# Kernel tuning notes

Measured on AMD Instinct MI355X. Metric: run time of the kernel, lower is better.

## Reference

```python
import jax, jax.numpy as jnp
import numpy as np

G = 128        # number of graphs
N = 512        # nodes per graph
F_IN = 128     # n_feat
H = 128        # agg_hidden
L = 5          # n_layer
FC = 128       # fc_hidden
C = 10         # n_class
E_HALF = 8192  # undirected edge pairs per graph (symmetrized -> 16384 directed)


def setup_inputs() -> dict:
    key = jax.random.key(0)
    ks = jax.random.split(key, 8)
    x = jax.random.normal(ks[0], (G * N, F_IN), dtype=jnp.float32)
    # per-graph random edges, offset into the block-diagonal node index space
    s = jax.random.randint(ks[1], (G, E_HALF), 0, N)
    d = jax.random.randint(ks[2], (G, E_HALF), 0, N)
    off = (jnp.arange(G) * N)[:, None]
    s = (s + off).reshape(-1)
    d = (d + off).reshape(-1)
    src = jnp.concatenate([s, d])  # symmetric adjacency (edges + reversed)
    dst = jnp.concatenate([d, s])
    eps = jnp.zeros((L,), jnp.float32)  # nn.Parameter(torch.zeros(n_layer))
    W = jax.random.normal(ks[3], (L, H, H), jnp.float32) / jnp.sqrt(H)
    b = jnp.zeros((L, H), jnp.float32)
    fc1_w = jax.random.normal(ks[4], (H, FC), jnp.float32) / jnp.sqrt(H)
    fc1_b = jnp.zeros((FC,), jnp.float32)
    fc2_w = jax.random.normal(ks[5], (FC, C), jnp.float32) / jnp.sqrt(FC)
    fc2_b = jnp.zeros((C,), jnp.float32)
    return {"x": x, "eps": eps, "W": W, "b": b,
            "fc1_w": fc1_w, "fc1_b": fc1_b, "fc2_w": fc2_w, "fc2_b": fc2_b,
            "src": src, "dst": dst}


def reference(x, eps, W, b, fc1_w, fc1_b, fc2_w, fc2_b, src, dst):
    n = x.shape[0]
    h = x
    for i in range(L):
        # sparse Adj @ h : gather along src, scatter-add to dst
        pooled = jax.ops.segment_sum(h[src], dst, num_segments=n)
        h = jax.nn.relu(((1.0 + eps[i]) * h + pooled) @ W[i] + b[i])
        # dropout p=0.0 / eval mode -> identity
    hg = h.reshape(G, N, -1).sum(axis=1)          # sum readout over nodes
    hg = jax.nn.relu(hg @ fc1_w + fc1_b)
    return jax.nn.softmax(hg @ fc2_w + fc2_b, axis=-1)
```

## Files before the change

kernel.cpp:

```cpp
#include <hip/hip_runtime.h>

#define GNUM  128
#define NPG   512
#define FDIM  128

#define OFF_A   0u
#define OFF_WT  (16u<<20)
#define OFF_HTA (17u<<20)
#define OFF_HTB (33u<<20)

typedef short bf16x8 __attribute__((ext_vector_type(8)));
typedef float f32x4  __attribute__((ext_vector_type(4)));
typedef unsigned short u16;

#define GLB_AS __attribute__((address_space(1)))
#define LDS_AS __attribute__((address_space(3)))

static __device__ inline void gload16(const void* g, void* l) {
    __builtin_amdgcn_global_load_lds((const GLB_AS unsigned*)g,
                                     (LDS_AS unsigned*)l, 16, 0, 0);
}

static __device__ inline unsigned bf1(float x) {
    unsigned b = __float_as_uint(x);
    return (b + 0x7fffu + ((b >> 16) & 1u)) >> 16;
}
static __device__ inline unsigned pack_bf2(float x, float y) {
    return bf1(x) | (bf1(y) << 16);
}
static __device__ inline bf16x8 cvt8n(unsigned x) {
    union { bf16x8 v; unsigned u[4]; } r;
#pragma unroll
    for (int i = 0; i < 4; ++i) {
        float f0 = (float)((x >> (8 * i)) & 0xFu);
        float f1 = (float)((x >> (8 * i + 4)) & 0xFu);
        r.u[i] = (__float_as_uint(f0) >> 16) | (__float_as_uint(f1) & 0xffff0000u);
    }
    return r.v;
}

__global__ __launch_bounds__(256) void k_prep(const float* __restrict__ x,
                                              u16* __restrict__ hT,
                                              const float* __restrict__ W,
                                              u16* __restrict__ wt) {
    __shared__ char Cs[128 * 144];
    int t = threadIdx.x;
    int bid = blockIdx.x;
    if (bid >= 1024) {
        int idx = (bid - 1024) * 256 + t;
        int l = idx >> 14, r = idx & 16383;
        int n = r >> 7, k = r & 127;
        wt[idx] = (u16)bf1(W[(l << 14) + k * 128 + n]);
        return;
    }
    int m0 = bid * 64;
    int g = m0 >> 9, ml0 = m0 & 511;
#pragma unroll
    for (int it = 0; it < 8; ++it) {
        int i = t + 256 * it;
        int nl = i >> 5, fq = i & 31;
        float4 v = *(const float4*)(x + (size_t)(m0 + nl) * FDIM + fq * 4);
        *(u16*)(Cs + (fq * 4 + 0) * 144 + nl * 2) = (u16)bf1(v.x);
        *(u16*)(Cs + (fq * 4 + 1) * 144 + nl * 2) = (u16)bf1(v.y);
        *(u16*)(Cs + (fq * 4 + 2) * 144 + nl * 2) = (u16)bf1(v.z);
        *(u16*)(Cs + (fq * 4 + 3) * 144 + nl * 2) = (u16)bf1(v.w);
    }
    __syncthreads();
    u16* hg = hT + (size_t)g * 65536 + ml0;
#pragma unroll
    for (int j = 0; j < 4; ++j) {
        int idx = t + 256 * j;
        int f = idx >> 3, piece = idx & 7;
        uint4 v = *(const uint4*)(Cs + f * 144 + piece * 16);
        *(uint4*)((char*)(hg + (size_t)f * 512) + piece * 16) = v;
    }
}

__global__ __launch_bounds__(1024) void k_adense(const int* __restrict__ src,
                                                 const int* __restrict__ dst,
                                                 unsigned* __restrict__ A4,
                                                 int halfE) {
    __shared__ uint4 cnt4[512 * 16];
    unsigned* cnt = (unsigned*)cnt4;
    int g = blockIdx.x;
    int t = threadIdx.x;
#pragma unroll
    for (int j = 0; j < 8; ++j) cnt4[t + 1024 * j] = make_uint4(0u, 0u, 0u, 0u);
    __syncthreads();
    int epg = halfE / GNUM;
#pragma unroll
    for (int r = 0; r < 2; ++r) {
        int base = r * halfE + g * epg;
        const int4* s4 = (const int4*)(src + base);
        const int4* d4 = (const int4*)(dst + base);
#pragma unroll
        for (int it = 0; it < 2; ++it) {
            int i = t + 1024 * it;
            int4 sv = s4[i], dv = d4[i];
            int s, d;
            s = sv.x & 511; d = dv.x & 511; atomicAdd(&cnt[d * 64 + (s >> 3)], 1u << ((s & 7) * 4));
            s = sv.y & 511; d = dv.y & 511; atomicAdd(&cnt[d * 64 + (s >> 3)], 1u << ((s & 7) * 4));
            s = sv.z & 511; d = dv.z & 511; atomicAdd(&cnt[d * 64 + (s >> 3)], 1u << ((s & 7) * 4));
            s = sv.w & 511; d = dv.w & 511; atomicAdd(&cnt[d * 64 + (s >> 3)], 1u << ((s & 7) * 4));
        }
    }
    __syncthreads();
    uint4* Ao = (uint4*)(A4 + (size_t)g * 512 * 64);
#pragma unroll
    for (int j = 0; j < 8; ++j) Ao[t + 1024 * j] = cnt4[t + 1024 * j];
}

__global__ __launch_bounds__(512, 2) void k_layer(const u16* __restrict__ hT,
                                                  u16* __restrict__ hTo,
                                                  const unsigned char* __restrict__ A,
                                                  const u16* __restrict__ wt,
                                                  const float* __restrict__ bias,
                                                  const float* __restrict__ eps) {
    __shared__ uint4 smem16[118784 / 16];
    char* smem = (char*)smem16;
    char* Ps = smem + 49152;
    int t = threadIdx.x;
    int w = t >> 6, lane = t & 63;
    int q = lane >> 4, ln = lane & 15;
    int g = blockIdx.x & 127, hf = blockIdx.x >> 7;
    const unsigned char* Ab = A + (size_t)g * 131072 + (size_t)hf * 65536;
    const u16* hb = hT + (size_t)g * 65536;
    int rA0 = w * 32 + ln;

    unsigned aA[32];
#pragma unroll
    for (int ch = 0; ch < 8; ++ch)
#pragma unroll
        for (int kcL = 0; kcL < 2; ++kcL)
#pragma unroll
            for (int h = 0; h < 2; ++h)
                aA[ch * 4 + kcL * 2 + h] = *(const unsigned*)
                    (Ab + (size_t)(rA0 + h * 16) * 256 + ch * 32 + kcL * 16 + q * 4);

    f32x4 acc[2][8];
#pragma unroll
    for (int mt = 0; mt < 2; ++mt)
#pragma unroll
        for (int nt = 0; nt < 8; ++nt) acc[mt][nt] = (f32x4){0.f, 0.f, 0.f, 0.f};

#pragma unroll
    for (int c = 0; c < 2; ++c)
#pragma unroll
        for (int j = 0; j < 2; ++j) {
            int p = t + 512 * j; int f = p >> 3;
            gload16((const char*)hb + (size_t)f * 1024 + c * 128
                        + (((p & 7) ^ (f & 7)) << 4),
                    smem + c * 16384 + p * 16);
        }
#pragma unroll
    for (int ch = 0; ch < 8; ++ch) {
        char* Bsc = smem + (ch % 3) * 16384;
        if (ch < 6) {
            int cn = ch + 2;
            char* Bsn = smem + (cn % 3) * 16384;
#pragma unroll
            for (int j = 0; j < 2; ++j) {
                int p = t + 512 * j; int f = p >> 3;
                gload16((const char*)hb + (size_t)f * 1024 + cn * 128
                            + (((p & 7) ^ (f & 7)) << 4),
                        Bsn + p * 16);
            }
        }
        if (ch < 6)      asm volatile("s_waitcnt vmcnt(4)" ::: "memory");
        else if (ch < 7) asm volatile("s_waitcnt vmcnt(2)" ::: "memory");
        else             asm volatile("s_waitcnt vmcnt(0)" ::: "memory");
        __builtin_amdgcn_s_barrier();
#pragma unroll
        for (int kcL = 0; kcL < 2; ++kcL) {
            bf16x8 af0 = cvt8n(aA[ch * 4 + kcL * 2 + 0]);
            bf16x8 af1 = cvt8n(aA[ch * 4 + kcL * 2 + 1]);
#pragma unroll
            for (int nt = 0; nt < 8; ++nt) {
                int f = nt * 16 + ln;
                int sB = f * 8 + ((kcL * 4 + q) ^ (f & 7));
                bf16x8 bf = *(const bf16x8*)(Bsc + sB * 16);
                acc[0][nt] = __builtin_amdgcn_mfma_f32_16x16x32_bf16(af0, bf, acc[0][nt], 0, 0, 0);
                acc[1][nt] = __builtin_amdgcn_mfma_f32_16x16x32_bf16(af1, bf, acc[1][nt], 0, 0, 0);
            }
        }
        __builtin_amdgcn_s_barrier();
    }
    float ep = 1.f + eps[0];
#pragma unroll
    for (int mt = 0; mt < 2; ++mt) {
        int rl0 = w * 32 + mt * 16 + q * 4;
        int mb0 = hf * 256 + rl0;
#pragma unroll
        for (int nt = 0; nt < 8; ++nt) {
            int f = nt * 16 + ln;
            uint2 sv = *(const uint2*)(hb + (size_t)f * 512 + mb0);
            float s0 = __uint_as_float(sv.x << 16);
            float s1 = __uint_as_float(sv.x & 0xffff0000u);
            float s2 = __uint_as_float(sv.y << 16);
            float s3 = __uint_as_float(sv.y & 0xffff0000u);
            f32x4 a = acc[mt][nt];
            *(u16*)(Ps + (rl0 + 0) * 272 + f * 2) = (u16)bf1(fmaf(ep, s0, a[0]));
            *(u16*)(Ps + (rl0 + 1) * 272 + f * 2) = (u16)bf1(fmaf(ep, s1, a[1]));
            *(u16*)(Ps + (rl0 + 2) * 272 + f * 2) = (u16)bf1(fmaf(ep, s2, a[2]));
            *(u16*)(Ps + (rl0 + 3) * 272 + f * 2) = (u16)bf1(fmaf(ep, s3, a[3]));
        }
    }
    __syncthreads();
    f32x4 acc2[2][8];
#pragma unroll
    for (int mt = 0; mt < 2; ++mt)
#pragma unroll
        for (int nt = 0; nt < 8; ++nt) acc2[mt][nt] = (f32x4){0.f, 0.f, 0.f, 0.f};
#pragma unroll
    for (int ks = 0; ks < 4; ++ks) {
        bf16x8 af0 = *(const bf16x8*)(Ps + rA0 * 272 + ks * 64 + q * 16);
        bf16x8 af1 = *(const bf16x8*)(Ps + (rA0 + 16) * 272 + ks * 64 + q * 16);
#pragma unroll
        for (int nt = 0; nt < 8; ++nt) {
            bf16x8 bf = *(const bf16x8*)(wt + (size_t)(nt * 16 + ln) * 128 + ks * 32 + q * 8);
            acc2[0][nt] = __builtin_amdgcn_mfma_f32_16x16x32_bf16(af0, bf, acc2[0][nt], 0, 0, 0);
            acc2[1][nt] = __builtin_amdgcn_mfma_f32_16x16x32_bf16(af1, bf, acc2[1][nt], 0, 0, 0);
        }
    }
    __syncthreads();
#pragma unroll
    for (int mt = 0; mt < 2; ++mt) {
        int rl0 = w * 32 + mt * 16 + q * 4;
#pragma unroll
        for (int nt = 0; nt < 8; ++nt) {
            int n = nt * 16 + ln;
            float bv = bias[n];
            f32x4 a = acc2[mt][nt];
            *(uint2*)(Ps + n * 528 + rl0 * 2) =
                make_uint2(pack_bf2(fmaxf(a[0] + bv, 0.f), fmaxf(a[1] + bv, 0.f)),
                           pack_bf2(fmaxf(a[2] + bv, 0.f), fmaxf(a[3] + bv, 0.f)));
        }
    }
    __syncthreads();
    u16* ho = hTo + (size_t)g * 65536 + hf * 256;
#pragma unroll
    for (int j = 0; j < 8; ++j) {
        int idx = t + 512 * j;
        int f = idx >> 5, piece = idx & 31;
        uint4 v = *(const uint4*)(Ps + f * 528 + piece * 16);
        *(uint4*)((char*)(ho + (size_t)f * 512) + piece * 16) = v;
    }
}

__global__ __launch_bounds__(128) void k_r(const u16* __restrict__ hT,
                                           const float* __restrict__ fc1w,
                                           const float* __restrict__ fc1b,
                                           const float* __restrict__ fc2w,
                                           const float* __restrict__ fc2b,
                                           float* __restrict__ out) {
    __shared__ float hg[128], z[128], lg[10];
    int g = blockIdx.x, t = threadIdx.x;
    const uint4* row = (const uint4*)(hT + (size_t)g * 65536 + (size_t)t * 512);
    float acc = 0.f;
#pragma unroll 4
    for (int i = 0; i < 64; ++i) {
        uint4 u = row[i];
        acc += __uint_as_float(u.x << 16) + __uint_as_float(u.x & 0xffff0000u);
        acc += __uint_as_float(u.y << 16) + __uint_as_float(u.y & 0xffff0000u);
        acc += __uint_as_float(u.z << 16) + __uint_as_float(u.z & 0xffff0000u);
        acc += __uint_as_float(u.w << 16) + __uint_as_float(u.w & 0xffff0000u);
    }
    hg[t] = acc;
    __syncthreads();
    float a1 = fc1b[t];
#pragma unroll 4
    for (int k = 0; k < 128; ++k) a1 = fmaf(hg[k], fc1w[k * 128 + t], a1);
    z[t] = fmaxf(a1, 0.f);
    __syncthreads();
    if (t < 10) {
        float l2 = fc2b[t];
        for (int k = 0; k < 128; ++k) l2 = fmaf(z[k], fc2w[k * 10 + t], l2);
        lg[t] = l2;
    }
    __syncthreads();
    if (t < 10) {
        float m = lg[0];
        for (int c = 1; c < 10; ++c) m = fmaxf(m, lg[c]);
        float ssum = 0.f;
        for (int c = 0; c < 10; ++c) ssum += expf(lg[c] - m);
        out[g * 10 + t] = expf(lg[t] - m) / ssum;
    }
}

extern "C" void kernel_launch(void* const* d_in, const int* in_sizes, int n_in,
                              void* d_out, int out_size, void* d_ws, size_t ws_size,
                              hipStream_t stream) {
    const float* x    = (const float*)d_in[0];
    const float* eps  = (const float*)d_in[1];
    const float* W    = (const float*)d_in[2];
    const float* b    = (const float*)d_in[3];
    const float* fc1w = (const float*)d_in[4];
    const float* fc1b = (const float*)d_in[5];
    const float* fc2w = (const float*)d_in[6];
    const float* fc2b = (const float*)d_in[7];
    const int*   src  = (const int*)d_in[8];
    const int*   dst  = (const int*)d_in[9];
    int E = in_sizes[8];
    int halfE = E >> 1;

    char* ws  = (char*)d_ws;
    unsigned char* Abuf = (unsigned char*)(ws + OFF_A);
    u16*  wtb = (u16*)(ws + OFF_WT);
    u16*  hta = (u16*)(ws + OFF_HTA);
    u16*  htb = (u16*)(ws + OFF_HTB);
    float* out = (float*)d_out;

    k_prep<<<1344, 256, 0, stream>>>(x, hta, W, wtb);
    k_adense<<<GNUM, 1024, 0, stream>>>(src, dst, (unsigned*)Abuf, halfE);

    u16* cur = hta;
    u16* nxt = htb;
    for (int l = 0; l < 5; ++l) {
        k_layer<<<GNUM * 2, 512, 0, stream>>>(cur, nxt, Abuf,
                                              wtb + l * 128 * 128, b + l * 128, eps + l);
        u16* tmp = cur; cur = nxt; nxt = tmp;
    }
    k_r<<<GNUM, 128, 0, stream>>>(cur, fc1w, fc1b, fc2w, fc2b, out);
}
```

Measured before the change: 282.6 us.

## Split layer kernel into quarter-graph blocks and read B operand directly from global

Each graph's layer is now handled by four 256-thread blocks covering 128 destination rows each, instead of two 512-thread blocks covering 256 rows. The LDS-staged triple-buffered async pipeline for the hT operand is dropped, and MFMA B fragments are loaded straight from global memory (relying on L2/L1 caching). This cuts LDS use from about 116 KB to 34 KB per block and removes the per-chunk barriers, allowing more blocks per CU. In exchange, each block re-reads the full per-graph feature tile from global memory, so the same data is fetched more times overall.

```diff
diff --git a/kernel.cpp b/kernel.cpp
--- a/kernel.cpp
+++ b/kernel.cpp
@@ -12,14 +12,6 @@
 typedef short bf16x8 __attribute__((ext_vector_type(8)));
 typedef float f32x4  __attribute__((ext_vector_type(4)));
 typedef unsigned short u16;
-
-#define GLB_AS __attribute__((address_space(1)))
-#define LDS_AS __attribute__((address_space(3)))
-
-static __device__ inline void gload16(const void* g, void* l) {
-    __builtin_amdgcn_global_load_lds((const GLB_AS unsigned*)g,
-                                     (LDS_AS unsigned*)l, 16, 0, 0);
-}
 
 static __device__ inline unsigned bf1(float x) {
     unsigned b = __float_as_uint(x);
@@ -110,20 +102,19 @@
     for (int j = 0; j < 8; ++j) Ao[t + 1024 * j] = cnt4[t + 1024 * j];
 }
 
-__global__ __launch_bounds__(512, 2) void k_layer(const u16* __restrict__ hT,
+__global__ __launch_bounds__(256, 2) void k_layer(const u16* __restrict__ hT,
                                                   u16* __restrict__ hTo,
                                                   const unsigned char* __restrict__ A,
                                                   const u16* __restrict__ wt,
                                                   const float* __restrict__ bias,
                                                   const float* __restrict__ eps) {
-    __shared__ uint4 smem16[118784 / 16];
-    char* smem = (char*)smem16;
-    char* Ps = smem + 49152;
+    __shared__ uint4 smem16[34816 / 16];
+    char* Ps = (char*)smem16;
     int t = threadIdx.x;
     int w = t >> 6, lane = t & 63;
     int q = lane >> 4, ln = lane & 15;
-    int g = blockIdx.x & 127, hf = blockIdx.x >> 7;
-    const unsigned char* Ab = A + (size_t)g * 131072 + (size_t)hf * 65536;
+    int g = blockIdx.x & 127, dq = blockIdx.x >> 7;
+    const unsigned char* Ab = A + (size_t)g * 131072 + (size_t)dq * 32768;
     const u16* hb = hT + (size_t)g * 65536;
     int rA0 = w * 32 + ln;
 
@@ -144,52 +135,30 @@
         for (int nt = 0; nt < 8; ++nt) acc[mt][nt] = (f32x4){0.f, 0.f, 0.f, 0.f};
 
 #pragma unroll
-    for (int c = 0; c < 2; ++c)
-#pragma unroll
-        for (int j = 0; j < 2; ++j) {
-            int p = t + 512 * j; int f = p >> 3;
-            gload16((const char*)hb + (size_t)f * 1024 + c * 128
-                        + (((p & 7) ^ (f & 7)) << 4),
-                    smem + c * 16384 + p * 16);
-        }
-#pragma unroll
     for (int ch = 0; ch < 8; ++ch) {
-        char* Bsc = smem + (ch % 3) * 16384;
-        if (ch < 6) {
-            int cn = ch + 2;
-            char* Bsn = smem + (cn % 3) * 16384;
-#pragma unroll
-            for (int j = 0; j < 2; ++j) {
-                int p = t + 512 * j; int f = p >> 3;
-                gload16((const char*)hb + (size_t)f * 1024 + cn * 128
-                            + (((p & 7) ^ (f & 7)) << 4),
-                        Bsn + p * 16);
+#pragma unroll
+        for (int kcL = 0; kcL < 2; ++kcL) {
+            bf16x8 bf[8];
+#pragma unroll
+            for (int nt = 0; nt < 8; ++nt) {
+                int f = nt * 16 + ln;
+                bf[nt] = *(const bf16x8*)(hb + (size_t)f * 512
+                                          + ch * 64 + kcL * 32 + q * 8);
             }
-        }
-        if (ch < 6)      asm volatile("s_waitcnt vmcnt(4)" ::: "memory");
-        else if (ch < 7) asm volatile("s_waitcnt vmcnt(2)" ::: "memory");
-        else             asm volatile("s_waitcnt vmcnt(0)" ::: "memory");
-        __builtin_amdgcn_s_barrier();
-#pragma unroll
-        for (int kcL = 0; kcL < 2; ++kcL) {
             bf16x8 af0 = cvt8n(aA[ch * 4 + kcL * 2 + 0]);
             bf16x8 af1 = cvt8n(aA[ch * 4 + kcL * 2 + 1]);
 #pragma unroll
             for (int nt = 0; nt < 8; ++nt) {
-                int f = nt * 16 + ln;
-                int sB = f * 8 + ((kcL * 4 + q) ^ (f & 7));
-                bf16x8 bf = *(const bf16x8*)(Bsc + sB * 16);
-                acc[0][nt] = __builtin_amdgcn_mfma_f32_16x16x32_bf16(af0, bf, acc[0][nt], 0, 0, 0);
-                acc[1][nt] = __builtin_amdgcn_mfma_f32_16x16x32_bf16(af1, bf, acc[1][nt], 0, 0, 0);
+                acc[0][nt] = __builtin_amdgcn_mfma_f32_16x16x32_bf16(af0, bf[nt], acc[0][nt], 0, 0, 0);
+                acc[1][nt] = __builtin_amdgcn_mfma_f32_16x16x32_bf16(af1, bf[nt], acc[1][nt], 0, 0, 0);
             }
         }
-        __builtin_amdgcn_s_barrier();
     }
     float ep = 1.f + eps[0];
 #pragma unroll
     for (int mt = 0; mt < 2; ++mt) {
         int rl0 = w * 32 + mt * 16 + q * 4;
-        int mb0 = hf * 256 + rl0;
+        int mb0 = dq * 128 + rl0;
 #pragma unroll
         for (int nt = 0; nt < 8; ++nt) {
             int f = nt * 16 + ln;
@@ -231,18 +200,18 @@
             int n = nt * 16 + ln;
             float bv = bias[n];
             f32x4 a = acc2[mt][nt];
-            *(uint2*)(Ps + n * 528 + rl0 * 2) =
+            *(uint2*)(Ps + n * 272 + rl0 * 2) =
                 make_uint2(pack_bf2(fmaxf(a[0] + bv, 0.f), fmaxf(a[1] + bv, 0.f)),
                            pack_bf2(fmaxf(a[2] + bv, 0.f), fmaxf(a[3] + bv, 0.f)));
         }
     }
     __syncthreads();
-    u16* ho = hTo + (size_t)g * 65536 + hf * 256;
+    u16* ho = hTo + (size_t)g * 65536 + dq * 128;
 #pragma unroll
     for (int j = 0; j < 8; ++j) {
-        int idx = t + 512 * j;
-        int f = idx >> 5, piece = idx & 31;
-        uint4 v = *(const uint4*)(Ps + f * 528 + piece * 16);
+        int idx = t + 256 * j;
+        int f = idx >> 4, piece = idx & 15;
+        uint4 v = *(const uint4*)(Ps + f * 272 + piece * 16);
         *(uint4*)((char*)(ho + (size_t)f * 512) + piece * 16) = v;
     }
 }
@@ -316,7 +285,7 @@
     u16* cur = hta;
     u16* nxt = htb;
     for (int l = 0; l < 5; ++l) {
-        k_layer<<<GNUM * 2, 512, 0, stream>>>(cur, nxt, Abuf,
+        k_layer<<<GNUM * 4, 256, 0, stream>>>(cur, nxt, Abuf,
                                               wtb + l * 128 * 128, b + l * 128, eps + l);
         u16* tmp = cur; cur = nxt; nxt = tmp;
     }
```

Result: slower. 397.5 us (+40.7%).

## Fuse all GIN layers and readout into one persistent kernel with per-graph counters

Applied to the files above, without the earlier changes.

Replaces the five per-layer launches and the readout launch with a single kernel. Each graph is handled by four blocks of 256 threads, each owning a quarter of the nodes, and the blocks sync between layers through per-graph atomic counters in workspace. The adjacency fragment stays in registers across all layers, and the readout plus MLP runs in the first block once all layers finish. This removes launch overhead and repeated A loads, but relies on all 512 blocks being co-resident for the spin-waits to make progress, and adds inter-block spin synchronisation with smaller blocks.

```diff
diff --git a/kernel.cpp b/kernel.cpp
--- a/kernel.cpp
+++ b/kernel.cpp
@@ -6,6 +6,7 @@
 
 #define OFF_A   0u
 #define OFF_WT  (16u<<20)
+#define OFF_CNT ((16u<<20)+(256u<<10))
 #define OFF_HTA (17u<<20)
 #define OFF_HTB (33u<<20)
 
@@ -79,11 +80,13 @@
 __global__ __launch_bounds__(1024) void k_adense(const int* __restrict__ src,
                                                  const int* __restrict__ dst,
                                                  unsigned* __restrict__ A4,
+                                                 unsigned* __restrict__ cnt,
                                                  int halfE) {
     __shared__ uint4 cnt4[512 * 16];
-    unsigned* cnt = (unsigned*)cnt4;
+    unsigned* c = (unsigned*)cnt4;
     int g = blockIdx.x;
     int t = threadIdx.x;
+    if (t < 8) cnt[g * 8 + t] = 0u;
 #pragma unroll
     for (int j = 0; j < 8; ++j) cnt4[t + 1024 * j] = make_uint4(0u, 0u, 0u, 0u);
     __syncthreads();
@@ -98,10 +101,10 @@
             int i = t + 1024 * it;
             int4 sv = s4[i], dv = d4[i];
             int s, d;
-            s = sv.x & 511; d = dv.x & 511; atomicAdd(&cnt[d * 64 + (s >> 3)], 1u << ((s & 7) * 4));
-            s = sv.y & 511; d = dv.y & 511; atomicAdd(&cnt[d * 64 + (s >> 3)], 1u << ((s & 7) * 4));
-            s = sv.z & 511; d = dv.z & 511; atomicAdd(&cnt[d * 64 + (s >> 3)], 1u << ((s & 7) * 4));
-            s = sv.w & 511; d = dv.w & 511; atomicAdd(&cnt[d * 64 + (s >> 3)], 1u << ((s & 7) * 4));
+            s = sv.x & 511; d = dv.x & 511; atomicAdd(&c[d * 64 + (s >> 3)], 1u << ((s & 7) * 4));
+            s = sv.y & 511; d = dv.y & 511; atomicAdd(&c[d * 64 + (s >> 3)], 1u << ((s & 7) * 4));
+            s = sv.z & 511; d = dv.z & 511; atomicAdd(&c[d * 64 + (s >> 3)], 1u << ((s & 7) * 4));
+            s = sv.w & 511; d = dv.w & 511; atomicAdd(&c[d * 64 + (s >> 3)], 1u << ((s & 7) * 4));
         }
     }
     __syncthreads();
@@ -110,21 +113,24 @@
     for (int j = 0; j < 8; ++j) Ao[t + 1024 * j] = cnt4[t + 1024 * j];
 }
 
-__global__ __launch_bounds__(512, 2) void k_layer(const u16* __restrict__ hT,
-                                                  u16* __restrict__ hTo,
-                                                  const unsigned char* __restrict__ A,
-                                                  const u16* __restrict__ wt,
-                                                  const float* __restrict__ bias,
-                                                  const float* __restrict__ eps) {
-    __shared__ uint4 smem16[118784 / 16];
+__global__ __launch_bounds__(256, 2) void k_gin(
+        u16* __restrict__ hta, u16* __restrict__ htb,
+        const unsigned char* __restrict__ A,
+        const u16* __restrict__ wt,
+        const float* __restrict__ bias,
+        const float* __restrict__ eps,
+        const float* __restrict__ fc1w, const float* __restrict__ fc1b,
+        const float* __restrict__ fc2w, const float* __restrict__ fc2b,
+        float* __restrict__ out,
+        unsigned* __restrict__ cnt) {
+    __shared__ uint4 smem16[49152 / 16];
     char* smem = (char*)smem16;
-    char* Ps = smem + 49152;
+    char* Ps = smem;
     int t = threadIdx.x;
     int w = t >> 6, lane = t & 63;
     int q = lane >> 4, ln = lane & 15;
-    int g = blockIdx.x & 127, hf = blockIdx.x >> 7;
-    const unsigned char* Ab = A + (size_t)g * 131072 + (size_t)hf * 65536;
-    const u16* hb = hT + (size_t)g * 65536;
+    int g = blockIdx.x & 127, dq = blockIdx.x >> 7;
+    const unsigned char* Ab = A + (size_t)g * 131072 + (size_t)dq * 32768;
     int rA0 = w * 32 + ln;
 
     unsigned aA[32];
@@ -137,153 +143,174 @@
                 aA[ch * 4 + kcL * 2 + h] = *(const unsigned*)
                     (Ab + (size_t)(rA0 + h * 16) * 256 + ch * 32 + kcL * 16 + q * 4);
 
-    f32x4 acc[2][8];
-#pragma unroll
-    for (int mt = 0; mt < 2; ++mt)
-#pragma unroll
-        for (int nt = 0; nt < 8; ++nt) acc[mt][nt] = (f32x4){0.f, 0.f, 0.f, 0.f};
-
-#pragma unroll
-    for (int c = 0; c < 2; ++c)
-#pragma unroll
-        for (int j = 0; j < 2; ++j) {
-            int p = t + 512 * j; int f = p >> 3;
-            gload16((const char*)hb + (size_t)f * 1024 + c * 128
-                        + (((p & 7) ^ (f & 7)) << 4),
-                    smem + c * 16384 + p * 16);
-        }
-#pragma unroll
-    for (int ch = 0; ch < 8; ++ch) {
-        char* Bsc = smem + (ch % 3) * 16384;
-        if (ch < 6) {
-            int cn = ch + 2;
-            char* Bsn = smem + (cn % 3) * 16384;
-#pragma unroll
-            for (int j = 0; j < 2; ++j) {
-                int p = t + 512 * j; int f = p >> 3;
-                gload16((const char*)hb + (size_t)f * 1024 + cn * 128
+    for (int l = 0; l < 5; ++l) {
+        const u16* hb = ((l & 1) ? htb : hta) + (size_t)g * 65536;
+        u16* ho = ((l & 1) ? hta : htb) + (size_t)g * 65536 + dq * 128;
+        const u16* wl = wt + l * 16384;
+        float ep = 1.f + eps[l];
+
+        f32x4 acc[2][8];
+#pragma unroll
+        for (int mt = 0; mt < 2; ++mt)
+#pragma unroll
+            for (int nt = 0; nt < 8; ++nt) acc[mt][nt] = (f32x4){0.f, 0.f, 0.f, 0.f};
+
+#pragma unroll
+        for (int c = 0; c < 2; ++c)
+#pragma unroll
+            for (int j = 0; j < 4; ++j) {
+                int p = t + 256 * j; int f = p >> 3;
+                gload16((const char*)hb + (size_t)f * 1024 + c * 128
                             + (((p & 7) ^ (f & 7)) << 4),
-                        Bsn + p * 16);
-            }
-        }
-        if (ch < 6)      asm volatile("s_waitcnt vmcnt(4)" ::: "memory");
-        else if (ch < 7) asm volatile("s_waitcnt vmcnt(2)" ::: "memory");
-        else             asm volatile("s_waitcnt vmcnt(0)" ::: "memory");
-        __builtin_amdgcn_s_barrier();
-#pragma unroll
-        for (int kcL = 0; kcL < 2; ++kcL) {
-            bf16x8 af0 = cvt8n(aA[ch * 4 + kcL * 2 + 0]);
-            bf16x8 af1 = cvt8n(aA[ch * 4 + kcL * 2 + 1]);
+                        smem + c * 16384 + p * 16);
+            }
+#pragma unroll
+        for (int ch = 0; ch < 8; ++ch) {
+            char* Bsc = smem + (ch % 3) * 16384;
+            if (ch < 6) {
+                int cn = ch + 2;
+                char* Bsn = smem + (cn % 3) * 16384;
+#pragma unroll
+                for (int j = 0; j < 4; ++j) {
+                    int p = t + 256 * j; int f = p >> 3;
+                    gload16((const char*)hb + (size_t)f * 1024 + cn * 128
+                                + (((p & 7) ^ (f & 7)) << 4),
+                            Bsn + p * 16);
+                }
+            }
+            if (ch < 6)      asm volatile("s_waitcnt vmcnt(8)" ::: "memory");
+            else if (ch < 7) asm volatile("s_waitcnt vmcnt(4)" ::: "memory");
+            else             asm volatile("s_waitcnt vmcnt(0)" ::: "memory");
+            __builtin_amdgcn_s_barrier();
+#pragma unroll
+            for (int kcL = 0; kcL < 2; ++kcL) {
+                bf16x8 af0 = cvt8n(aA[ch * 4 + kcL * 2 + 0]);
+                bf16x8 af1 = cvt8n(aA[ch * 4 + kcL * 2 + 1]);
+#pragma unroll
+                for (int nt = 0; nt < 8; ++nt) {
+                    int f = nt * 16 + ln;
+                    int sB = f * 8 + ((kcL * 4 + q) ^ (f & 7));
+                    bf16x8 bf = *(const bf16x8*)(Bsc + sB * 16);
+                    acc[0][nt] = __builtin_amdgcn_mfma_f32_16x16x32_bf16(af0, bf, acc[0][nt], 0, 0, 0);
+                    acc[1][nt] = __builtin_amdgcn_mfma_f32_16x16x32_bf16(af1, bf, acc[1][nt], 0, 0, 0);
+                }
+            }
+            __builtin_amdgcn_s_barrier();
+        }
+#pragma unroll
+        for (int mt = 0; mt < 2; ++mt) {
+            int rl0 = w * 32 + mt * 16 + q * 4;
+            int mb0 = dq * 128 + rl0;
 #pragma unroll
             for (int nt = 0; nt < 8; ++nt) {
                 int f = nt * 16 + ln;
-                int sB = f * 8 + ((kcL * 4 + q) ^ (f & 7));
-                bf16x8 bf = *(const bf16x8*)(Bsc + sB * 16);
+                uint2 sv = *(const uint2*)(hb + (size_t)f * 512 + mb0);
+                float s0 = __uint_as_float(sv.x << 16);
+                float s1 = __uint_as_float(sv.x & 0xffff0000u);
+                float s2 = __uint_as_float(sv.y << 16);
+                float s3 = __uint_as_float(sv.y & 0xffff0000u);
+                f32x4 a = acc[mt][nt];
+                *(u16*)(Ps + (rl0 + 0) * 272 + f * 2) = (u16)bf1(fmaf(ep, s0, a[0]));
+                *(u16*)(Ps + (rl0 + 1) * 272 + f * 2) = (u16)bf1(fmaf(ep, s1, a[1]));
+                *(u16*)(Ps + (rl0 + 2) * 272 + f * 2) = (u16)bf1(fmaf(ep, s2, a[2]));
+                *(u16*)(Ps + (rl0 + 3) * 272 + f * 2) = (u16)bf1(fmaf(ep, s3, a[3]));
+            }
+        }
+        __syncthreads();
+#pragma unroll
+        for (int mt = 0; mt < 2; ++mt)
+#pragma unroll
+            for (int nt = 0; nt < 8; ++nt) acc[mt][nt] = (f32x4){0.f, 0.f, 0.f, 0.f};
+#pragma unroll
+        for (int ks = 0; ks < 4; ++ks) {
+            bf16x8 af0 = *(const bf16x8*)(Ps + rA0 * 272 + ks * 64 + q * 16);
+            bf16x8 af1 = *(const bf16x8*)(Ps + (rA0 + 16) * 272 + ks * 64 + q * 16);
+#pragma unroll
+            for (int nt = 0; nt < 8; ++nt) {
+                bf16x8 bf = *(const bf16x8*)(wl + (size_t)(nt * 16 + ln) * 128 + ks * 32 + q * 8);
                 acc[0][nt] = __builtin_amdgcn_mfma_f32_16x16x32_bf16(af0, bf, acc[0][nt], 0, 0, 0);
                 acc[1][nt] = __builtin_amdgcn_mfma_f32_16x16x32_bf16(af1, bf, acc[1][nt], 0, 0, 0);
             }
         }
-        __builtin_amdgcn_s_barrier();
-    }
-    float ep = 1.f + eps[0];
-#pragma unroll
-    for (int mt = 0; mt < 2; ++mt) {
-        int rl0 = w * 32 + mt * 16 + q * 4;
-        int mb0 = hf * 256 + rl0;
-#pragma unroll
-        for (int nt = 0; nt < 8; ++nt) {
-            int f = nt * 16 + ln;
-            uint2 sv = *(const uint2*)(hb + (size_t)f * 512 + mb0);
-            float s0 = __uint_as_float(sv.x << 16);
-            float s1 = __uint_as_float(sv.x & 0xffff0000u);
-            float s2 = __uint_as_float(sv.y << 16);
-            float s3 = __uint_as_float(sv.y & 0xffff0000u);
-            f32x4 a = acc[mt][nt];
-            *(u16*)(Ps + (rl0 + 0) * 272 + f * 2) = (u16)bf1(fmaf(ep, s0, a[0]));
-            *(u16*)(Ps + (rl0 + 1) * 272 + f * 2) = (u16)bf1(fmaf(ep, s1, a[1]));
-            *(u16*)(Ps + (rl0 + 2) * 272 + f * 2) = (u16)bf1(fmaf(ep, s2, a[2]));
-            *(u16*)(Ps + (rl0 + 3) * 272 + f * 2) = (u16)bf1(fmaf(ep, s3, a[3]));
-        }
-    }
-    __syncthreads();
-    f32x4 acc2[2][8];
-#pragma unroll
-    for (int mt = 0; mt < 2; ++mt)
-#pragma unroll
-        for (int nt = 0; nt < 8; ++nt) acc2[mt][nt] = (f32x4){0.f, 0.f, 0.f, 0.f};
-#pragma unroll
-    for (int ks = 0; ks < 4; ++ks) {
-        bf16x8 af0 = *(const bf16x8*)(Ps + rA0 * 272 + ks * 64 + q * 16);
-        bf16x8 af1 = *(const bf16x8*)(Ps + (rA0 + 16) * 272 + ks * 64 + q * 16);
-#pragma unroll
-        for (int nt = 0; nt < 8; ++nt) {
-            bf16x8 bf = *(const bf16x8*)(wt + (size_t)(nt * 16 + ln) * 128 + ks * 32 + q * 8);
-            acc2[0][nt] = __builtin_amdgcn_mfma_f32_16x16x32_bf16(af0, bf, acc2[0][nt], 0, 0, 0);
-            acc2[1][nt] = __builtin_amdgcn_mfma_f32_16x16x32_bf16(af1, bf, acc2[1][nt], 0, 0, 0);
-        }
-    }
-    __syncthreads();
-#pragma unroll
-    for (int mt = 0; mt < 2; ++mt) {
-        int rl0 = w * 32 + mt * 16 + q * 4;
-#pragma unroll
-        for (int nt = 0; nt < 8; ++nt) {
-            int n = nt * 16 + ln;
-            float bv = bias[n];
-            f32x4 a = acc2[mt][nt];
-            *(uint2*)(Ps + n * 528 + rl0 * 2) =
-                make_uint2(pack_bf2(fmaxf(a[0] + bv, 0.f), fmaxf(a[1] + bv, 0.f)),
-                           pack_bf2(fmaxf(a[2] + bv, 0.f), fmaxf(a[3] + bv, 0.f)));
-        }
-    }
-    __syncthreads();
-    u16* ho = hTo + (size_t)g * 65536 + hf * 256;
-#pragma unroll
-    for (int j = 0; j < 8; ++j) {
-        int idx = t + 512 * j;
-        int f = idx >> 5, piece = idx & 31;
-        uint4 v = *(const uint4*)(Ps + f * 528 + piece * 16);
-        *(uint4*)((char*)(ho + (size_t)f * 512) + piece * 16) = v;
-    }
-}
-
-__global__ __launch_bounds__(128) void k_r(const u16* __restrict__ hT,
-                                           const float* __restrict__ fc1w,
-                                           const float* __restrict__ fc1b,
-                                           const float* __restrict__ fc2w,
-                                           const float* __restrict__ fc2b,
-                                           float* __restrict__ out) {
-    __shared__ float hg[128], z[128], lg[10];
-    int g = blockIdx.x, t = threadIdx.x;
-    const uint4* row = (const uint4*)(hT + (size_t)g * 65536 + (size_t)t * 512);
-    float acc = 0.f;
+        __syncthreads();
+#pragma unroll
+        for (int mt = 0; mt < 2; ++mt) {
+            int rl0 = w * 32 + mt * 16 + q * 4;
+#pragma unroll
+            for (int nt = 0; nt < 8; ++nt) {
+                int n = nt * 16 + ln;
+                float bv = bias[l * 128 + n];
+                f32x4 a = acc[mt][nt];
+                *(uint2*)(Ps + n * 272 + rl0 * 2) =
+                    make_uint2(pack_bf2(fmaxf(a[0] + bv, 0.f), fmaxf(a[1] + bv, 0.f)),
+                               pack_bf2(fmaxf(a[2] + bv, 0.f), fmaxf(a[3] + bv, 0.f)));
+            }
+        }
+        __syncthreads();
+#pragma unroll
+        for (int j = 0; j < 8; ++j) {
+            int idx = t + 256 * j;
+            int f = idx >> 4, piece = idx & 15;
+            uint4 v = *(const uint4*)(Ps + f * 272 + piece * 16);
+            *(uint4*)((char*)(ho + (size_t)f * 512) + piece * 16) = v;
+        }
+        __threadfence();
+        if (t == 0)
+            __hip_atomic_fetch_add(&cnt[g * 8 + l], 1u,
+                                   __ATOMIC_RELEASE, __HIP_MEMORY_SCOPE_AGENT);
+        if (l < 4) {
+            if (t == 0)
+                while (__hip_atomic_load(&cnt[g * 8 + l],
+                                         __ATOMIC_ACQUIRE, __HIP_MEMORY_SCOPE_AGENT) < 4u)
+                    __builtin_amdgcn_s_sleep(1);
+            __syncthreads();
+        }
+    }
+
+    if (dq == 0) {
+        if (t == 0)
+            while (__hip_atomic_load(&cnt[g * 8 + 4],
+                                     __ATOMIC_ACQUIRE, __HIP_MEMORY_SCOPE_AGENT) < 4u)
+                __builtin_amdgcn_s_sleep(1);
+        __syncthreads();
+        float* hg = (float*)smem;
+        float* zz = hg + 128;
+        float* lg = zz + 128;
+        const u16* hf = htb + (size_t)g * 65536;
+        if (t < 128) {
+            const uint4* row = (const uint4*)(hf + (size_t)t * 512);
+            float acc = 0.f;
 #pragma unroll 4
-    for (int i = 0; i < 64; ++i) {
-        uint4 u = row[i];
-        acc += __uint_as_float(u.x << 16) + __uint_as_float(u.x & 0xffff0000u);
-        acc += __uint_as_float(u.y << 16) + __uint_as_float(u.y & 0xffff0000u);
-        acc += __uint_as_float(u.z << 16) + __uint_as_float(u.z & 0xffff0000u);
-        acc += __uint_as_float(u.w << 16) + __uint_as_float(u.w & 0xffff0000u);
-    }
-    hg[t] = acc;
-    __syncthreads();
-    float a1 = fc1b[t];
+            for (int i = 0; i < 64; ++i) {
+                uint4 u = row[i];
+                acc += __uint_as_float(u.x << 16) + __uint_as_float(u.x & 0xffff0000u);
+                acc += __uint_as_float(u.y << 16) + __uint_as_float(u.y & 0xffff0000u);
+                acc += __uint_as_float(u.z << 16) + __uint_as_float(u.z & 0xffff0000u);
+                acc += __uint_as_float(u.w << 16) + __uint_as_float(u.w & 0xffff0000u);
+            }
+            hg[t] = acc;
+        }
+        __syncthreads();
+        if (t < 128) {
+            float a1 = fc1b[t];
 #pragma unroll 4
-    for (int k = 0; k < 128; ++k) a1 = fmaf(hg[k], fc1w[k * 128 + t], a1);
-    z[t] = fmaxf(a1, 0.f);
-    __syncthreads();
-    if (t < 10) {
-        float l2 = fc2b[t];
-        for (int k = 0; k < 128; ++k) l2 = fmaf(z[k], fc2w[k * 10 + t], l2);
-        lg[t] = l2;
-    }
-    __syncthreads();
-    if (t < 10) {
-        float m = lg[0];
-        for (int c = 1; c < 10; ++c) m = fmaxf(m, lg[c]);
-        float ssum = 0.f;
-        for (int c = 0; c < 10; ++c) ssum += expf(lg[c] - m);
-        out[g * 10 + t] = expf(lg[t] - m) / ssum;
+            for (int k = 0; k < 128; ++k) a1 = fmaf(hg[k], fc1w[k * 128 + t], a1);
+            zz[t] = fmaxf(a1, 0.f);
+        }
+        __syncthreads();
+        if (t < 10) {
+            float l2 = fc2b[t];
+            for (int k = 0; k < 128; ++k) l2 = fmaf(zz[k], fc2w[k * 10 + t], l2);
+            lg[t] = l2;
+        }
+        __syncthreads();
+        if (t < 10) {
+            float m = lg[0];
+            for (int c = 1; c < 10; ++c) m = fmaxf(m, lg[c]);
+            float ssum = 0.f;
+            for (int c = 0; c < 10; ++c) ssum += expf(lg[c] - m);
+            out[g * 10 + t] = expf(lg[t] - m) / ssum;
+        }
     }
 }
 
@@ -306,19 +333,13 @@
     char* ws  = (char*)d_ws;
     unsigned char* Abuf = (unsigned char*)(ws + OFF_A);
     u16*  wtb = (u16*)(ws + OFF_WT);
+    unsigned* cnt = (unsigned*)(ws + OFF_CNT);
     u16*  hta = (u16*)(ws + OFF_HTA);
     u16*  htb = (u16*)(ws + OFF_HTB);
     float* out = (float*)d_out;
 
     k_prep<<<1344, 256, 0, stream>>>(x, hta, W, wtb);
-    k_adense<<<GNUM, 1024, 0, stream>>>(src, dst, (unsigned*)Abuf, halfE);
-
-    u16* cur = hta;
-    u16* nxt = htb;
-    for (int l = 0; l < 5; ++l) {
-        k_layer<<<GNUM * 2, 512, 0, stream>>>(cur, nxt, Abuf,
-                                              wtb + l * 128 * 128, b + l * 128, eps + l);
-        u16* tmp = cur; cur = nxt; nxt = tmp;
-    }
-    k_r<<<GNUM, 128, 0, stream>>>(cur, fc1w, fc1b, fc2w, fc2b, out);
-}
+    k_adense<<<GNUM, 1024, 0, stream>>>(src, dst, (unsigned*)Abuf, cnt, halfE);
+    k_gin<<<GNUM * 4, 256, 0, stream>>>(hta, htb, Abuf, wtb, b, eps,
+                                        fc1w, fc1b, fc2w, fc2b, out, cnt);
+}
```

Result: slower. 682.1 us (+141.4%).
